# Kernel optimization log

Hardware: AMD Instinct MI355X
Metric: run time of the kernel (lower is better)

The kernel has to match this reference:

```python
import jax, jax.numpy as jnp
import numpy as np

B, SQ, ST, SI = 8, 4096, 77, 16
C, DC, H = 1280, 2048, 20
DH = C // H  # 64
SCALE = 1.0 / np.sqrt(DH).astype(np.float32)
SCALE_ID = 1.0
SCALE_HAIR = 1.0


def setup_inputs() -> dict:
    key = jax.random.key(0)
    ks = jax.random.split(key, 12)
    std = 0.02
    return {
        "hidden_states": jax.random.normal(ks[0], (B, SQ, C), jnp.float32),
        "text_states": jax.random.normal(ks[1], (B, ST, DC), jnp.float32),
        "id_states": jax.random.normal(ks[2], (B, SI, DC), jnp.float32),
        "hair_states": jax.random.normal(ks[3], (B, SI, DC), jnp.float32),
        # weights stored as [in, out] (transpose of torch nn.Linear layout)
        "Wq": jax.random.normal(ks[4], (C, C), jnp.float32) * std,
        "Wk": jax.random.normal(ks[5], (DC, C), jnp.float32) * std,
        "Wv": jax.random.normal(ks[6], (DC, C), jnp.float32) * std,
        "Wo": jax.random.normal(ks[7], (C, C), jnp.float32) * std,
        "b_o": jnp.zeros((C,), jnp.float32),
        "Wk_id": jax.random.normal(ks[8], (DC, C), jnp.float32) * std,
        "Wv_id": jax.random.normal(ks[9], (DC, C), jnp.float32) * std,
        "Wk_hair": jax.random.normal(ks[10], (DC, C), jnp.float32) * std,
        "Wv_hair": jax.random.normal(ks[11], (DC, C), jnp.float32) * std,
    }


def _heads(x):
    # [B, S, C] -> [B, H, S, DH]
    b, s, _ = x.shape
    return x.reshape(b, s, H, DH).transpose(0, 2, 1, 3)


def _merge(x):
    # [B, H, S, DH] -> [B, S, C]
    b, h, s, d = x.shape
    return x.transpose(0, 2, 1, 3).reshape(b, s, h * d)


def _attend(q, k, v):
    # q: [B,H,Sq,DH], k/v: [B,H,Sk,DH]; fp32 scores (attn_fp32=True)
    scores = jnp.einsum("bhqd,bhkd->bhqk", q.astype(jnp.float32), k.astype(jnp.float32)) * SCALE
    p = jax.nn.softmax(scores, axis=-1)
    return jnp.einsum("bhqk,bhkd->bhqd", p, v.astype(jnp.float32))


def reference(hidden_states, text_states, id_states, hair_states, Wq, Wk, Wv, Wo, b_o, Wk_id, Wv_id, Wk_hair, Wv_hair):
    q = _heads(hidden_states @ Wq)
    # base cross-attention to text (standard diffusers AttnProcessor)
    base = _attend(q, _heads(text_states @ Wk), _heads(text_states @ Wv))
    result = _merge(base) @ Wo + b_o
    # ID branch: own K/V projections, shared query and to_out
    out_id = _attend(q, _heads(id_states @ Wk_id), _heads(id_states @ Wv_id))
    result = result + SCALE_ID * (_merge(out_id) @ Wo + b_o)
    # hair branch
    out_h = _attend(q, _heads(hair_states @ Wk_hair), _heads(hair_states @ Wv_hair))
    result = result + SCALE_HAIR * (_merge(out_h) @ Wo + b_o)
    return result
```

## Files before the change

kernel.cpp:

```cpp
#include <hip/hip_runtime.h>
#include <cstdint>
#include <cstddef>

typedef unsigned short u16;
typedef __attribute__((ext_vector_type(4))) float     f32x4_t;
typedef __attribute__((ext_vector_type(8))) __bf16    bf16x8_t;
typedef __attribute__((ext_vector_type(8))) u16       u16x8_t;
typedef __attribute__((ext_vector_type(4))) u16       u16x4_t;
typedef __attribute__((ext_vector_type(4))) float     fvec4_t;

#define DEVI __device__ __forceinline__

constexpr int Bn  = 8;
constexpr int SQn = 4096;
constexpr int STn = 77;
constexpr int SIn = 16;
constexpr int Cn  = 1280;
constexpr int DCn = 2048;
constexpr int Hn  = 20;
constexpr float SCALEf = 0.125f;
constexpr float L2E    = 1.4426950408889634f;

typedef const __attribute__((address_space(1))) void* gas_t;
typedef __attribute__((address_space(3))) void*       las_t;

DEVI u16 f2bf(float f) {
  union { float f; unsigned u; } cv; cv.f = f;
  unsigned u = cv.u;
  return (u16)((u + 0x7FFFu + ((u >> 16) & 1u)) >> 16);
}

__global__ __launch_bounds__(256) void cast_bf16_kernel(
    const float* __restrict__ src, u16* __restrict__ dst, int n8) {
  int i = blockIdx.x * 256 + threadIdx.x;
  if (i >= n8) return;
  const fvec4_t* s4 = (const fvec4_t*)src;
  fvec4_t a = s4[2 * i], b = s4[2 * i + 1];
  u16x8_t o;
  o[0] = f2bf(a[0]); o[1] = f2bf(a[1]); o[2] = f2bf(a[2]); o[3] = f2bf(a[3]);
  o[4] = f2bf(b[0]); o[5] = f2bf(b[1]); o[6] = f2bf(b[2]); o[7] = f2bf(b[3]);
  ((u16x8_t*)dst)[i] = o;
}

struct TrArgs {
  const float* src[8];
  u16*         dst[8];
  int          Kd[8];
};

__global__ __launch_bounds__(256) void transpose_cast_kernel(TrArgs ta) {
  int z = blockIdx.z;
  int K = ta.Kd[z];
  int k0 = blockIdx.x * 32;
  if (k0 >= K) return;
  int n0 = blockIdx.y * 32;
  __shared__ float tile[32][33];
  int tx = threadIdx.x & 31, ty = threadIdx.x >> 5;
  const float* src = ta.src[z];
#pragma unroll
  for (int i = 0; i < 4; i++) {
    int r = ty + 8 * i;
    tile[r][tx] = src[(size_t)(k0 + r) * Cn + n0 + tx];
  }
  __syncthreads();
  u16* dst = ta.dst[z];
#pragma unroll
  for (int i = 0; i < 4; i++) {
    int r = ty + 8 * i;
    dst[(size_t)(n0 + r) * K + k0 + tx] = f2bf(tile[tx][r]);
  }
}

template <int OUT_F32>
__global__ __launch_bounds__(512, 2) void gemm256_kernel(
    const u16* __restrict__ A, const u16* __restrict__ Bt,
    void* __restrict__ Cout, const float* __restrict__ bias, int M, int K) {
  __shared__ __align__(16) u16 lds[2][2][256 * 64];
  const int t = threadIdx.x;
  const int w = t >> 6, l = t & 63;
  const int wr = w >> 2, wc = w & 3;
  const int lr = l & 15;
  const int m0 = blockIdx.x * 256, n0 = blockIdx.y * 256;
  const int NT = K >> 6;

  f32x4_t acc[8][4];
#pragma unroll
  for (int am = 0; am < 8; am++)
#pragma unroll
    for (int an = 0; an < 4; an++) {
      f32x4_t z = {0.f, 0.f, 0.f, 0.f};
      acc[am][an] = z;
    }

  auto stagePart = [&](int cb, int kt, int i) {
    const int k0 = kt * 64;
    int row = i * 64 + w * 8 + (l >> 3);
    int col16 = (l & 7) ^ (row & 7);
    const u16* ga = A + (size_t)(m0 + row) * K + k0 + col16 * 8;
    __builtin_amdgcn_global_load_lds((gas_t)ga, (las_t)(&lds[cb][0][0] + (size_t)(i * 512 + w * 64) * 8), 16, 0, 0);
    const u16* gb = Bt + (size_t)(n0 + row) * K + k0 + col16 * 8;
    __builtin_amdgcn_global_load_lds((gas_t)gb, (las_t)(&lds[cb][1][0] + (size_t)(i * 512 + w * 64) * 8), 16, 0, 0);
  };
  auto readB = [&](bf16x8_t (&dst)[2][2], const u16* bB, int qn) {
#pragma unroll
    for (int n = 0; n < 2; n++) {
      int row = wc * 64 + qn * 32 + n * 16 + lr;
#pragma unroll
      for (int kk = 0; kk < 2; kk++) {
        int slot = kk * 4 + (l >> 4);
        dst[n][kk] = *(const bf16x8_t*)&bB[row * 64 + ((slot ^ (row & 7)) * 8)];
      }
    }
  };
  auto readA = [&](bf16x8_t (&dst)[4][2], const u16* bA, int qm) {
#pragma unroll
    for (int m = 0; m < 4; m++) {
      int row = wr * 128 + qm * 64 + m * 16 + lr;
#pragma unroll
      for (int kk = 0; kk < 2; kk++) {
        int slot = kk * 4 + (l >> 4);
        dst[m][kk] = *(const bf16x8_t*)&bA[row * 64 + ((slot ^ (row & 7)) * 8)];
      }
    }
  };
  auto mfma16 = [&](bf16x8_t (&Af)[4][2], bf16x8_t (&Bf)[2][2], int qm, int qn) {
    __builtin_amdgcn_s_setprio(1);
#pragma unroll
    for (int m = 0; m < 4; m++)
#pragma unroll
      for (int n = 0; n < 2; n++) {
        acc[qm * 4 + m][qn * 2 + n] = __builtin_amdgcn_mfma_f32_16x16x32_bf16(
            Af[m][0], Bf[n][0], acc[qm * 4 + m][qn * 2 + n], 0, 0, 0);
        acc[qm * 4 + m][qn * 2 + n] = __builtin_amdgcn_mfma_f32_16x16x32_bf16(
            Af[m][1], Bf[n][1], acc[qm * 4 + m][qn * 2 + n], 0, 0, 0);
      }
    __builtin_amdgcn_s_setprio(0);
  };

#pragma unroll
  for (int i = 0; i < 4; i++) stagePart(0, 0, i);
#pragma unroll
  for (int i = 0; i < 4; i++) stagePart(1, 1, i);
  asm volatile("s_waitcnt vmcnt(8)" ::: "memory");
  __builtin_amdgcn_sched_barrier(0);
  __builtin_amdgcn_s_barrier();

  for (int kt = 0; kt < NT; kt++) {
    const int cb = kt & 1;
    const u16* bA = &lds[cb][0][0];
    const u16* bB = &lds[cb][1][0];
    const bool st = (kt + 2 < NT);
    bf16x8_t Ar[4][2], B0[2][2], B1[2][2];

    readB(B0, bB, 0);
    readA(Ar, bA, 0);
    __builtin_amdgcn_s_barrier();
    asm volatile("s_waitcnt lgkmcnt(0)" ::: "memory");
    __builtin_amdgcn_sched_barrier(0);
    mfma16(Ar, B0, 0, 0);
    __builtin_amdgcn_s_barrier();

    readB(B1, bB, 1);
    __builtin_amdgcn_s_barrier();
    asm volatile("s_waitcnt lgkmcnt(0)" ::: "memory");
    __builtin_amdgcn_sched_barrier(0);
    mfma16(Ar, B1, 0, 1);
    __builtin_amdgcn_s_barrier();

    readA(Ar, bA, 1);
    __builtin_amdgcn_s_barrier();
    if (st) { stagePart(cb, kt + 2, 0); stagePart(cb, kt + 2, 1); }
    asm volatile("s_waitcnt lgkmcnt(0)" ::: "memory");
    __builtin_amdgcn_sched_barrier(0);
    mfma16(Ar, B0, 1, 0);
    __builtin_amdgcn_s_barrier();

    if (st) { stagePart(cb, kt + 2, 2); stagePart(cb, kt + 2, 3); }
    mfma16(Ar, B1, 1, 1);

    if (st) {
      asm volatile("s_waitcnt vmcnt(8)" ::: "memory");
    } else if (kt + 1 < NT) {
      asm volatile("s_waitcnt vmcnt(0)" ::: "memory");
    }
    __builtin_amdgcn_sched_barrier(0);
    __builtin_amdgcn_s_barrier();
  }

#pragma unroll
  for (int am = 0; am < 8; am++) {
    int rbase = m0 + wr * 128 + am * 16 + (l >> 4) * 4;
#pragma unroll
    for (int an = 0; an < 4; an++) {
      int col = n0 + wc * 64 + an * 16 + lr;
#pragma unroll
      for (int j = 0; j < 4; j++) {
        int r = rbase + j;
        if (OUT_F32) {
          ((float*)Cout)[(size_t)r * Cn + col] = acc[am][an][j] + 3.0f * bias[col];
        } else {
          ((u16*)Cout)[(size_t)r * Cn + col] = f2bf(acc[am][an][j]);
        }
      }
    }
  }
}

DEVI void gemm_body(const u16* __restrict__ A, const u16* __restrict__ Bt,
                    u16* __restrict__ Cout, int M, int K, int mtile, int ntile) {
  __shared__ __align__(16) u16 lA[128 * 64];
  __shared__ __align__(16) u16 lB[128 * 64];
  const int t = threadIdx.x;
  const int w = t >> 6, l = t & 63;
  const int wr = w >> 1, wc = w & 1;
  const int m0 = mtile * 128, n0 = ntile * 128;
  const int lr = l & 15, lk = (l >> 4) * 8;

  f32x4_t acc[4][4];
#pragma unroll
  for (int m = 0; m < 4; m++)
#pragma unroll
    for (int n = 0; n < 4; n++) {
      f32x4_t z = {0.f, 0.f, 0.f, 0.f};
      acc[m][n] = z;
    }

  for (int k0 = 0; k0 < K; k0 += 64) {
    __syncthreads();
#pragma unroll
    for (int i = 0; i < 4; i++) {
      int c = i * 256 + t;
      int row = c >> 3, ch = c & 7;
      int rA = m0 + row;
      rA = rA < M ? rA : M - 1;
      const u16* ga = A + (size_t)rA * K + k0 + ch * 8;
      __builtin_amdgcn_global_load_lds((gas_t)ga, (las_t)&lA[(i * 256 + w * 64) * 8], 16, 0, 0);
      const u16* gb = Bt + (size_t)(n0 + row) * K + k0 + ch * 8;
      __builtin_amdgcn_global_load_lds((gas_t)gb, (las_t)&lB[(i * 256 + w * 64) * 8], 16, 0, 0);
    }
    __syncthreads();
#pragma unroll
    for (int kk = 0; kk < 2; kk++) {
      bf16x8_t af[4], bf[4];
#pragma unroll
      for (int m = 0; m < 4; m++)
        af[m] = *(const bf16x8_t*)&lA[(64 * wr + 16 * m + lr) * 64 + kk * 32 + lk];
#pragma unroll
      for (int n = 0; n < 4; n++)
        bf[n] = *(const bf16x8_t*)&lB[(64 * wc + 16 * n + lr) * 64 + kk * 32 + lk];
#pragma unroll
      for (int m = 0; m < 4; m++)
#pragma unroll
        for (int n = 0; n < 4; n++)
          acc[m][n] = __builtin_amdgcn_mfma_f32_16x16x32_bf16(af[m], bf[n], acc[m][n], 0, 0, 0);
    }
  }

  const int rj = (l >> 4) * 4;
#pragma unroll
  for (int m = 0; m < 4; m++) {
    int rbase = m0 + 64 * wr + 16 * m + rj;
#pragma unroll
    for (int n = 0; n < 4; n++) {
      int col = n0 + 64 * wc + 16 * n + lr;
#pragma unroll
      for (int j = 0; j < 4; j++) {
        int r = rbase + j;
        if (r < M) ((u16*)Cout)[(size_t)r * Cn + col] = f2bf(acc[m][n][j]);
      }
    }
  }
}

struct KV6 {
  const u16* A[6];
  const u16* Bt[6];
  u16*       Cp[6];
  int        M[6];
};

__global__ __launch_bounds__(256) void gemm_kv_kernel(KV6 kv) {
  int z = blockIdx.z;
  int M = kv.M[z];
  if ((int)blockIdx.x * 128 >= M) return;
  gemm_body(kv.A[z], kv.Bt[z], kv.Cp[z], M, DCn, blockIdx.x, blockIdx.y);
}

__global__ __launch_bounds__(512, 4) void attn_kernel(
    const u16* __restrict__ q,
    const u16* __restrict__ ktx, const u16* __restrict__ vtx,
    const u16* __restrict__ kid, const u16* __restrict__ vid,
    const u16* __restrict__ kh,  const u16* __restrict__ vh,
    u16* __restrict__ osum) {
  __shared__ __align__(16) u16 KP[8 * 16 * 136];
  __shared__ __align__(16) u16 Vt[64 * 128];

  const int t = threadIdx.x, w = t >> 6, l = t & 63;
  const int bh = blockIdx.y, b = bh / Hn, h = bh % Hn;
  const int lr = l & 15, lk = (l >> 4) * 8;

  for (int i = t; i < 112 * 8; i += 512) {
    int row = i >> 3, ch = i & 7;
    u16x8_t vv;
#pragma unroll
    for (int x = 0; x < 8; x++) vv[x] = 0;
    if (row < 77)
      vv = *(const u16x8_t*)(ktx + (size_t)(b * STn + row) * Cn + h * 64 + ch * 8);
    else if (row >= 80 && row < 96)
      vv = *(const u16x8_t*)(kid + (size_t)(b * SIn + row - 80) * Cn + h * 64 + ch * 8);
    else if (row >= 96)
      vv = *(const u16x8_t*)(kh + (size_t)(b * SIn + row - 96) * Cn + h * 64 + ch * 8);
    *(u16x8_t*)&KP[row * 72 + ch * 8] = vv;
  }
  for (int i = t; i < 128 * 8; i += 512) {
    int key = i >> 3, ch = i & 7;
    u16x8_t vv;
#pragma unroll
    for (int x = 0; x < 8; x++) vv[x] = 0;
    if (key < 77)
      vv = *(const u16x8_t*)(vtx + (size_t)(b * STn + key) * Cn + h * 64 + ch * 8);
    else if (key >= 80 && key < 96)
      vv = *(const u16x8_t*)(vid + (size_t)(b * SIn + key - 80) * Cn + h * 64 + ch * 8);
    else if (key >= 96 && key < 112)
      vv = *(const u16x8_t*)(vh + (size_t)(b * SIn + key - 96) * Cn + h * 64 + ch * 8);
    int G = key >> 3, wk = key & 7;
#pragma unroll
    for (int x = 0; x < 8; x++) {
      int d = ch * 8 + x;
      int Gs = G ^ x ^ ch;
      Vt[d * 128 + Gs * 8 + wk] = vv[x];
    }
  }
  __syncthreads();

  bf16x8_t kf[7][2];
#pragma unroll
  for (int tt = 0; tt < 7; tt++)
#pragma unroll
    for (int kk = 0; kk < 2; kk++)
      kf[tt][kk] = *(const bf16x8_t*)&KP[(tt * 16 + lr) * 72 + kk * 32 + lk];
  __syncthreads();

  u16* Pw = &KP[w * 16 * 136];
  {
    u16x4_t z4; z4[0] = 0; z4[1] = 0; z4[2] = 0; z4[3] = 0;
    *(u16x4_t*)&Pw[(l >> 2) * 136 + 112 + (l & 3) * 4] = z4;
  }

  for (int rt = 0; rt < 4; rt++) {
    const int s0 = blockIdx.x * 512 + w * 64 + rt * 16;
    bf16x8_t qf[2];
#pragma unroll
    for (int kk = 0; kk < 2; kk++)
      qf[kk] = *(const bf16x8_t*)&q[(size_t)(b * SQn + s0 + lr) * Cn + h * 64 + kk * 32 + lk];

    f32x4_t sc[7];
#pragma unroll
    for (int tt = 0; tt < 7; tt++) {
      f32x4_t z = {0.f, 0.f, 0.f, 0.f};
      z = __builtin_amdgcn_mfma_f32_16x16x32_bf16(qf[0], kf[tt][0], z, 0, 0, 0);
      z = __builtin_amdgcn_mfma_f32_16x16x32_bf16(qf[1], kf[tt][1], z, 0, 0, 0);
      sc[tt] = z;
    }
#pragma unroll
    for (int tt = 0; tt < 7; tt++)
#pragma unroll
      for (int j = 0; j < 4; j++) sc[tt][j] *= SCALEf;
    if (lr >= 13) {
#pragma unroll
      for (int j = 0; j < 4; j++) sc[4][j] = -3.0e38f;
    }

    float mx[4], sm[4], inv[4];

#pragma unroll
    for (int j = 0; j < 4; j++) {
      float m = sc[0][j];
      m = fmaxf(m, sc[1][j]); m = fmaxf(m, sc[2][j]);
      m = fmaxf(m, sc[3][j]); m = fmaxf(m, sc[4][j]);
      mx[j] = m;
    }
#pragma unroll
    for (int d = 1; d < 16; d <<= 1)
#pragma unroll
      for (int j = 0; j < 4; j++) mx[j] = fmaxf(mx[j], __shfl_xor(mx[j], d));
#pragma unroll
    for (int j = 0; j < 4; j++) sm[j] = 0.f;
#pragma unroll
    for (int tt = 0; tt < 5; tt++)
#pragma unroll
      for (int j = 0; j < 4; j++) {
        float p = __builtin_amdgcn_exp2f((sc[tt][j] - mx[j]) * L2E);
        sc[tt][j] = p;
        sm[j] += p;
      }
#pragma unroll
    for (int d = 1; d < 16; d <<= 1)
#pragma unroll
      for (int j = 0; j < 4; j++) sm[j] += __shfl_xor(sm[j], d);
#pragma unroll
    for (int j = 0; j < 4; j++) inv[j] = __builtin_amdgcn_rcpf(sm[j]);
#pragma unroll
    for (int tt = 0; tt < 5; tt++)
#pragma unroll
      for (int j = 0; j < 4; j++) {
        __bf16 pb = (__bf16)(sc[tt][j] * inv[j]);
        Pw[((l >> 4) * 4 + j) * 136 + tt * 16 + lr] = *(u16*)&pb;
      }

#pragma unroll
    for (int j = 0; j < 4; j++) mx[j] = sc[5][j];
#pragma unroll
    for (int d = 1; d < 16; d <<= 1)
#pragma unroll
      for (int j = 0; j < 4; j++) mx[j] = fmaxf(mx[j], __shfl_xor(mx[j], d));
#pragma unroll
    for (int j = 0; j < 4; j++) {
      float p = __builtin_amdgcn_exp2f((sc[5][j] - mx[j]) * L2E);
      sc[5][j] = p;
      sm[j] = p;
    }
#pragma unroll
    for (int d = 1; d < 16; d <<= 1)
#pragma unroll
      for (int j = 0; j < 4; j++) sm[j] += __shfl_xor(sm[j], d);
#pragma unroll
    for (int j = 0; j < 4; j++) {
      __bf16 pb = (__bf16)(sc[5][j] * __builtin_amdgcn_rcpf(sm[j]));
      Pw[((l >> 4) * 4 + j) * 136 + 80 + lr] = *(u16*)&pb;
    }

#pragma unroll
    for (int j = 0; j < 4; j++) mx[j] = sc[6][j];
#pragma unroll
    for (int d = 1; d < 16; d <<= 1)
#pragma unroll
      for (int j = 0; j < 4; j++) mx[j] = fmaxf(mx[j], __shfl_xor(mx[j], d));
#pragma unroll
    for (int j = 0; j < 4; j++) {
      float p = __builtin_amdgcn_exp2f((sc[6][j] - mx[j]) * L2E);
      sc[6][j] = p;
      sm[j] = p;
    }
#pragma unroll
    for (int d = 1; d < 16; d <<= 1)
#pragma unroll
      for (int j = 0; j < 4; j++) sm[j] += __shfl_xor(sm[j], d);
#pragma unroll
    for (int j = 0; j < 4; j++) {
      __bf16 pb = (__bf16)(sc[6][j] * __builtin_amdgcn_rcpf(sm[j]));
      Pw[((l >> 4) * 4 + j) * 136 + 96 + lr] = *(u16*)&pb;
    }

    f32x4_t oacc[4];
#pragma unroll
    for (int n = 0; n < 4; n++) {
      f32x4_t z = {0.f, 0.f, 0.f, 0.f};
      oacc[n] = z;
    }
#pragma unroll
    for (int ktile = 0; ktile < 4; ktile++) {
      bf16x8_t pf = *(const bf16x8_t*)&Pw[lr * 136 + ktile * 32 + lk];
#pragma unroll
      for (int n = 0; n < 4; n++) {
        int d = 16 * n + lr;
        int Gs = (4 * ktile + (l >> 4)) ^ (d & 7) ^ ((d >> 3) & 7);
        bf16x8_t vf = *(const bf16x8_t*)&Vt[d * 128 + Gs * 8];
        oacc[n] = __builtin_amdgcn_mfma_f32_16x16x32_bf16(pf, vf, oacc[n], 0, 0, 0);
      }
    }
#pragma unroll
    for (int n = 0; n < 4; n++)
#pragma unroll
      for (int j = 0; j < 4; j++) {
        int srow = s0 + (l >> 4) * 4 + j;
        __bf16 ob = (__bf16)oacc[n][j];
        osum[(size_t)(b * SQn + srow) * Cn + h * 64 + 16 * n + lr] = *(u16*)&ob;
      }
  }
}

extern "C" void kernel_launch(void* const* d_in, const int* in_sizes, int n_in,
                              void* d_out, int out_size, void* d_ws, size_t ws_size,
                              hipStream_t stream) {
  (void)in_sizes; (void)n_in; (void)out_size; (void)ws_size;
  const float* hidden  = (const float*)d_in[0];
  const float* text    = (const float*)d_in[1];
  const float* ids     = (const float*)d_in[2];
  const float* hair    = (const float*)d_in[3];
  const float* Wq      = (const float*)d_in[4];
  const float* Wk      = (const float*)d_in[5];
  const float* Wv      = (const float*)d_in[6];
  const float* Wo      = (const float*)d_in[7];
  const float* b_o     = (const float*)d_in[8];
  const float* Wk_id   = (const float*)d_in[9];
  const float* Wv_id   = (const float*)d_in[10];
  const float* Wk_hair = (const float*)d_in[11];
  const float* Wv_hair = (const float*)d_in[12];
  float* out = (float*)d_out;

  char* ws = (char*)d_ws;
  size_t off = 0;
  auto carve = [&](size_t bytes) -> char* {
    char* p = ws + off;
    off += (bytes + 255) & ~(size_t)255;
    return p;
  };

  u16* h_bf    = (u16*)carve((size_t)Bn * SQn * Cn * 2);
  u16* q_bf    = (u16*)carve((size_t)Bn * SQn * Cn * 2);
  u16* text_bf = (u16*)carve((size_t)Bn * STn * DCn * 2);
  u16* id_bf   = (u16*)carve((size_t)Bn * SIn * DCn * 2);
  u16* hair_bf = (u16*)carve((size_t)Bn * SIn * DCn * 2);
  u16* Wq_t    = (u16*)carve((size_t)Cn * Cn * 2);
  u16* Wo_t    = (u16*)carve((size_t)Cn * Cn * 2);
  u16* Wk_t    = (u16*)carve((size_t)DCn * Cn * 2);
  u16* Wv_t    = (u16*)carve((size_t)DCn * Cn * 2);
  u16* Wkid_t  = (u16*)carve((size_t)DCn * Cn * 2);
  u16* Wvid_t  = (u16*)carve((size_t)DCn * Cn * 2);
  u16* Wkh_t   = (u16*)carve((size_t)DCn * Cn * 2);
  u16* Wvh_t   = (u16*)carve((size_t)DCn * Cn * 2);
  u16* k_text  = (u16*)carve((size_t)Bn * STn * Cn * 2);
  u16* v_text  = (u16*)carve((size_t)Bn * STn * Cn * 2);
  u16* k_id    = (u16*)carve((size_t)Bn * SIn * Cn * 2);
  u16* v_id    = (u16*)carve((size_t)Bn * SIn * Cn * 2);
  u16* k_hr    = (u16*)carve((size_t)Bn * SIn * Cn * 2);
  u16* v_hr    = (u16*)carve((size_t)Bn * SIn * Cn * 2);
  u16* attn_sum = h_bf;

  {
    int n8 = Bn * SQn * Cn / 8;
    cast_bf16_kernel<<<dim3((n8 + 255) / 256), 256, 0, stream>>>(hidden, h_bf, n8);
  }
  {
    int n8 = Bn * STn * DCn / 8;
    cast_bf16_kernel<<<dim3((n8 + 255) / 256), 256, 0, stream>>>(text, text_bf, n8);
  }
  {
    int n8 = Bn * SIn * DCn / 8;
    cast_bf16_kernel<<<dim3((n8 + 255) / 256), 256, 0, stream>>>(ids, id_bf, n8);
    cast_bf16_kernel<<<dim3((n8 + 255) / 256), 256, 0, stream>>>(hair, hair_bf, n8);
  }

  {
    TrArgs ta;
    ta.src[0] = Wq;      ta.dst[0] = Wq_t;   ta.Kd[0] = Cn;
    ta.src[1] = Wo;      ta.dst[1] = Wo_t;   ta.Kd[1] = Cn;
    ta.src[2] = Wk;      ta.dst[2] = Wk_t;   ta.Kd[2] = DCn;
    ta.src[3] = Wv;      ta.dst[3] = Wv_t;   ta.Kd[3] = DCn;
    ta.src[4] = Wk_id;   ta.dst[4] = Wkid_t; ta.Kd[4] = DCn;
    ta.src[5] = Wv_id;   ta.dst[5] = Wvid_t; ta.Kd[5] = DCn;
    ta.src[6] = Wk_hair; ta.dst[6] = Wkh_t;  ta.Kd[6] = DCn;
    ta.src[7] = Wv_hair; ta.dst[7] = Wvh_t;  ta.Kd[7] = DCn;
    transpose_cast_kernel<<<dim3(DCn / 32, Cn / 32, 8), 256, 0, stream>>>(ta);
  }

  gemm256_kernel<0><<<dim3(Bn * SQn / 256, Cn / 256), 512, 0, stream>>>(
      h_bf, Wq_t, q_bf, nullptr, Bn * SQn, Cn);

  {
    KV6 kv;
    kv.A[0] = text_bf; kv.Bt[0] = Wk_t;   kv.Cp[0] = k_text; kv.M[0] = Bn * STn;
    kv.A[1] = text_bf; kv.Bt[1] = Wv_t;   kv.Cp[1] = v_text; kv.M[1] = Bn * STn;
    kv.A[2] = id_bf;   kv.Bt[2] = Wkid_t; kv.Cp[2] = k_id;   kv.M[2] = Bn * SIn;
    kv.A[3] = id_bf;   kv.Bt[3] = Wvid_t; kv.Cp[3] = v_id;   kv.M[3] = Bn * SIn;
    kv.A[4] = hair_bf; kv.Bt[4] = Wkh_t;  kv.Cp[4] = k_hr;   kv.M[4] = Bn * SIn;
    kv.A[5] = hair_bf; kv.Bt[5] = Wvh_t;  kv.Cp[5] = v_hr;   kv.M[5] = Bn * SIn;
    gemm_kv_kernel<<<dim3((Bn * STn + 127) / 128, Cn / 128, 6), 256, 0, stream>>>(kv);
  }

  attn_kernel<<<dim3(SQn / 512, Bn * Hn), 512, 0, stream>>>(
      q_bf, k_text, v_text, k_id, v_id, k_hr, v_hr, attn_sum);

  gemm256_kernel<1><<<dim3(Bn * SQn / 256, Cn / 256), 512, 0, stream>>>(
      attn_sum, Wo_t, out, b_o, Bn * SQn, Cn);
}
```

Baseline: 533.8 us.

## Store Q, K, V and attention output in head-major layout

Q, K and V projections now write their outputs in [B,H,S,64] head-major order. The attention kernel reads and writes contiguous per-(batch,head) slabs instead of 128-byte strided slices of 1280-wide rows. The output GEMM reads its A operand straight from the head-major buffer, using the k-tile index as the head index. This is meant to improve memory coalescing in attention, at the cost of scattered 2-byte stores in the GEMM epilogues.

```diff
diff --git a/kernel.cpp b/kernel.cpp
--- a/kernel.cpp
+++ b/kernel.cpp
@@ -71,7 +71,7 @@
   }
 }
 
-template <int OUT_F32>
+template <int OUT_MODE, int A_HM>
 __global__ __launch_bounds__(512, 2) void gemm256_kernel(
     const u16* __restrict__ A, const u16* __restrict__ Bt,
     void* __restrict__ Cout, const float* __restrict__ bias, int M, int K) {
@@ -96,7 +96,13 @@
     const int k0 = kt * 64;
     int row = i * 64 + w * 8 + (l >> 3);
     int col16 = (l & 7) ^ (row & 7);
-    const u16* ga = A + (size_t)(m0 + row) * K + k0 + col16 * 8;
+    const u16* ga;
+    if (A_HM) {
+      int gr = m0 + row, bb = gr >> 12, ss = gr & 4095;
+      ga = A + (((size_t)bb * Hn + kt) * SQn + ss) * 64 + col16 * 8;
+    } else {
+      ga = A + (size_t)(m0 + row) * K + k0 + col16 * 8;
+    }
     __builtin_amdgcn_global_load_lds((gas_t)ga, (las_t)(&lds[cb][0][0] + (size_t)(i * 512 + w * 64) * 8), 16, 0, 0);
     const u16* gb = Bt + (size_t)(n0 + row) * K + k0 + col16 * 8;
     __builtin_amdgcn_global_load_lds((gas_t)gb, (las_t)(&lds[cb][1][0] + (size_t)(i * 512 + w * 64) * 8), 16, 0, 0);
@@ -196,10 +202,12 @@
 #pragma unroll
       for (int j = 0; j < 4; j++) {
         int r = rbase + j;
-        if (OUT_F32) {
+        if (OUT_MODE == 1) {
           ((float*)Cout)[(size_t)r * Cn + col] = acc[am][an][j] + 3.0f * bias[col];
         } else {
-          ((u16*)Cout)[(size_t)r * Cn + col] = f2bf(acc[am][an][j]);
+          int bb = r >> 12, ss = r & 4095;
+          int hh = (n0 >> 6) + wc, dd = an * 16 + lr;
+          ((u16*)Cout)[(((size_t)bb * Hn + hh) * SQn + ss) * 64 + dd] = f2bf(acc[am][an][j]);
         }
       }
     }
@@ -207,7 +215,7 @@
 }
 
 DEVI void gemm_body(const u16* __restrict__ A, const u16* __restrict__ Bt,
-                    u16* __restrict__ Cout, int M, int K, int mtile, int ntile) {
+                    u16* __restrict__ Cout, int M, int S, int K, int mtile, int ntile) {
   __shared__ __align__(16) u16 lA[128 * 64];
   __shared__ __align__(16) u16 lB[128 * 64];
   const int t = threadIdx.x;
@@ -257,16 +265,20 @@
   }
 
   const int rj = (l >> 4) * 4;
+  const int hh = ntile * 2 + wc;
 #pragma unroll
   for (int m = 0; m < 4; m++) {
     int rbase = m0 + 64 * wr + 16 * m + rj;
 #pragma unroll
     for (int n = 0; n < 4; n++) {
-      int col = n0 + 64 * wc + 16 * n + lr;
+      int dd = 16 * n + lr;
 #pragma unroll
       for (int j = 0; j < 4; j++) {
         int r = rbase + j;
-        if (r < M) ((u16*)Cout)[(size_t)r * Cn + col] = f2bf(acc[m][n][j]);
+        if (r < M) {
+          int bb = r / S, ss = r - bb * S;
+          Cout[(((size_t)bb * Hn + hh) * S + ss) * 64 + dd] = f2bf(acc[m][n][j]);
+        }
       }
     }
   }
@@ -277,13 +289,14 @@
   const u16* Bt[6];
   u16*       Cp[6];
   int        M[6];
+  int        S[6];
 };
 
 __global__ __launch_bounds__(256) void gemm_kv_kernel(KV6 kv) {
   int z = blockIdx.z;
   int M = kv.M[z];
   if ((int)blockIdx.x * 128 >= M) return;
-  gemm_body(kv.A[z], kv.Bt[z], kv.Cp[z], M, DCn, blockIdx.x, blockIdx.y);
+  gemm_body(kv.A[z], kv.Bt[z], kv.Cp[z], M, kv.S[z], DCn, blockIdx.x, blockIdx.y);
 }
 
 __global__ __launch_bounds__(512, 4) void attn_kernel(
@@ -299,17 +312,27 @@
   const int bh = blockIdx.y, b = bh / Hn, h = bh % Hn;
   const int lr = l & 15, lk = (l >> 4) * 8;
 
+  const u16* qB   = q   + ((size_t)bh) * SQn * 64;
+  const u16* ktxB = ktx + ((size_t)bh) * STn * 64;
+  const u16* vtxB = vtx + ((size_t)bh) * STn * 64;
+  const u16* kidB = kid + ((size_t)bh) * SIn * 64;
+  const u16* vidB = vid + ((size_t)bh) * SIn * 64;
+  const u16* khB  = kh  + ((size_t)bh) * SIn * 64;
+  const u16* vhB  = vh  + ((size_t)bh) * SIn * 64;
+  u16*       oB   = osum + ((size_t)bh) * SQn * 64;
+  (void)b; (void)h;
+
   for (int i = t; i < 112 * 8; i += 512) {
     int row = i >> 3, ch = i & 7;
     u16x8_t vv;
 #pragma unroll
     for (int x = 0; x < 8; x++) vv[x] = 0;
     if (row < 77)
-      vv = *(const u16x8_t*)(ktx + (size_t)(b * STn + row) * Cn + h * 64 + ch * 8);
+      vv = *(const u16x8_t*)(ktxB + (size_t)row * 64 + ch * 8);
     else if (row >= 80 && row < 96)
-      vv = *(const u16x8_t*)(kid + (size_t)(b * SIn + row - 80) * Cn + h * 64 + ch * 8);
+      vv = *(const u16x8_t*)(kidB + (size_t)(row - 80) * 64 + ch * 8);
     else if (row >= 96)
-      vv = *(const u16x8_t*)(kh + (size_t)(b * SIn + row - 96) * Cn + h * 64 + ch * 8);
+      vv = *(const u16x8_t*)(khB + (size_t)(row - 96) * 64 + ch * 8);
     *(u16x8_t*)&KP[row * 72 + ch * 8] = vv;
   }
   for (int i = t; i < 128 * 8; i += 512) {
@@ -318,11 +341,11 @@
 #pragma unroll
     for (int x = 0; x < 8; x++) vv[x] = 0;
     if (key < 77)
-      vv = *(const u16x8_t*)(vtx + (size_t)(b * STn + key) * Cn + h * 64 + ch * 8);
+      vv = *(const u16x8_t*)(vtxB + (size_t)key * 64 + ch * 8);
     else if (key >= 80 && key < 96)
-      vv = *(const u16x8_t*)(vid + (size_t)(b * SIn + key - 80) * Cn + h * 64 + ch * 8);
+      vv = *(const u16x8_t*)(vidB + (size_t)(key - 80) * 64 + ch * 8);
     else if (key >= 96 && key < 112)
-      vv = *(const u16x8_t*)(vh + (size_t)(b * SIn + key - 96) * Cn + h * 64 + ch * 8);
+      vv = *(const u16x8_t*)(vhB + (size_t)(key - 96) * 64 + ch * 8);
     int G = key >> 3, wk = key & 7;
 #pragma unroll
     for (int x = 0; x < 8; x++) {
@@ -352,7 +375,7 @@
     bf16x8_t qf[2];
 #pragma unroll
     for (int kk = 0; kk < 2; kk++)
-      qf[kk] = *(const bf16x8_t*)&q[(size_t)(b * SQn + s0 + lr) * Cn + h * 64 + kk * 32 + lk];
+      qf[kk] = *(const bf16x8_t*)&qB[(size_t)(s0 + lr) * 64 + kk * 32 + lk];
 
     f32x4_t sc[7];
 #pragma unroll
@@ -475,7 +498,7 @@
       for (int j = 0; j < 4; j++) {
         int srow = s0 + (l >> 4) * 4 + j;
         __bf16 ob = (__bf16)oacc[n][j];
-        osum[(size_t)(b * SQn + srow) * Cn + h * 64 + 16 * n + lr] = *(u16*)&ob;
+        oB[(size_t)srow * 64 + 16 * n + lr] = *(u16*)&ob;
       }
   }
 }
@@ -555,23 +578,23 @@
     transpose_cast_kernel<<<dim3(DCn / 32, Cn / 32, 8), 256, 0, stream>>>(ta);
   }
 
-  gemm256_kernel<0><<<dim3(Bn * SQn / 256, Cn / 256), 512, 0, stream>>>(
+  gemm256_kernel<2, 0><<<dim3(Bn * SQn / 256, Cn / 256), 512, 0, stream>>>(
       h_bf, Wq_t, q_bf, nullptr, Bn * SQn, Cn);
 
   {
     KV6 kv;
-    kv.A[0] = text_bf; kv.Bt[0] = Wk_t;   kv.Cp[0] = k_text; kv.M[0] = Bn * STn;
-    kv.A[1] = text_bf; kv.Bt[1] = Wv_t;   kv.Cp[1] = v_text; kv.M[1] = Bn * STn;
-    kv.A[2] = id_bf;   kv.Bt[2] = Wkid_t; kv.Cp[2] = k_id;   kv.M[2] = Bn * SIn;
-    kv.A[3] = id_bf;   kv.Bt[3] = Wvid_t; kv.Cp[3] = v_id;   kv.M[3] = Bn * SIn;
-    kv.A[4] = hair_bf; kv.Bt[4] = Wkh_t;  kv.Cp[4] = k_hr;   kv.M[4] = Bn * SIn;
-    kv.A[5] = hair_bf; kv.Bt[5] = Wvh_t;  kv.Cp[5] = v_hr;   kv.M[5] = Bn * SIn;
+    kv.A[0] = text_bf; kv.Bt[0] = Wk_t;   kv.Cp[0] = k_text; kv.M[0] = Bn * STn; kv.S[0] = STn;
+    kv.A[1] = text_bf; kv.Bt[1] = Wv_t;   kv.Cp[1] = v_text; kv.M[1] = Bn * STn; kv.S[1] = STn;
+    kv.A[2] = id_bf;   kv.Bt[2] = Wkid_t; kv.Cp[2] = k_id;   kv.M[2] = Bn * SIn; kv.S[2] = SIn;
+    kv.A[3] = id_bf;   kv.Bt[3] = Wvid_t; kv.Cp[3] = v_id;   kv.M[3] = Bn * SIn; kv.S[3] = SIn;
+    kv.A[4] = hair_bf; kv.Bt[4] = Wkh_t;  kv.Cp[4] = k_hr;   kv.M[4] = Bn * SIn; kv.S[4] = SIn;
+    kv.A[5] = hair_bf; kv.Bt[5] = Wvh_t;  kv.Cp[5] = v_hr;   kv.M[5] = Bn * SIn; kv.S[5] = SIn;
     gemm_kv_kernel<<<dim3((Bn * STn + 127) / 128, Cn / 128, 6), 256, 0, stream>>>(kv);
   }
 
   attn_kernel<<<dim3(SQn / 512, Bn * Hn), 512, 0, stream>>>(
       q_bf, k_text, v_text, k_id, v_id, k_hr, v_hr, attn_sum);
 
-  gemm256_kernel<1><<<dim3(Bn * SQn / 256, Cn / 256), 512, 0, stream>>>(
+  gemm256_kernel<1, 1><<<dim3(Bn * SQn / 256, Cn / 256), 512, 0, stream>>>(
       attn_sum, Wo_t, out, b_o, Bn * SQn, Cn);
 }
```

New measurement: 553.6 us. 1.04x slower.
